# Kernel optimization log

Hardware: AMD Instinct MI355X
Metric: run time of the kernel (lower is better)

## Reference

```python
import jax, jax.numpy as jnp
import numpy as np
import math

N = 50000          # nodes
E = 800000         # edges (~avg degree 16)
G = 2048           # graphs
NUM_RBF = 128
CUTOFF = 5.0       # max_radius
C_RAD = 16         # radial channels
SH_DIM = 9         # 1x0e+1x1e+1x2e
_AVG_DEGREE = 15.57930850982666
_AVG_NUM_NODES = 18.03065905448718


def spherical_harmonics_l012(vec):
    """e3nn spherical harmonics l=0,1,2, normalize=True, component normalization."""
    r = jnp.linalg.norm(vec, axis=-1, keepdims=True)
    u = vec / jnp.maximum(r, 1e-12)
    x, y, z = u[..., 0], u[..., 1], u[..., 2]
    s3, s5, s15 = math.sqrt(3.0), math.sqrt(5.0), math.sqrt(15.0)
    x2, y2, z2 = x * x, y * y, z * z
    return jnp.stack([
        jnp.ones_like(x),                 # l=0
        s3 * x, s3 * y, s3 * z,           # l=1
        s15 * x * z,                      # l=2 (e3nn ordering)
        s15 * x * y,
        s5 * (y2 - 0.5 * (x2 + z2)),
        s15 * y * z,
        (s15 / 2.0) * (z2 - x2),
    ], axis=-1)


def exp_normal_smearing(dist):
    """ExpNormalSmearing with cutoff_lower=0, cutoff_upper=CUTOFF, num_rbf=NUM_RBF."""
    alpha = 5.0 / CUTOFF
    start = math.exp(-CUTOFF)
    means = jnp.linspace(start, 1.0, NUM_RBF).astype(dist.dtype)
    beta = (2.0 / NUM_RBF * (1.0 - start)) ** (-2)
    d = dist[..., None]
    cut = 0.5 * (jnp.cos(d * math.pi / CUTOFF) + 1.0) * (d < CUTOFF).astype(d.dtype)
    return cut * jnp.exp(-beta * (jnp.exp(-alpha * d) - means) ** 2)


def setup_inputs() -> dict:
    key = jax.random.key(0)
    ks = jax.random.split(key, 16)
    s = 0.05
    return {
        "pos": jax.random.normal(ks[0], (N, 3), jnp.float32) * 2.0,
        "atom_table": jax.random.normal(ks[1], (64, C_RAD * SH_DIM), jnp.float32) * s,
        "W1": jax.random.normal(ks[2], (NUM_RBF, 64), jnp.float32) * s,
        "b1": jnp.zeros((64,), jnp.float32),
        "W2": jax.random.normal(ks[3], (64, 64), jnp.float32) * s,
        "b2": jnp.zeros((64,), jnp.float32),
        "W3": jax.random.normal(ks[4], (64, C_RAD), jnp.float32) * s,
        "Wh1": jax.random.normal(ks[5], (C_RAD * SH_DIM, C_RAD * SH_DIM), jnp.float32) * s,
        "bh1": jnp.zeros((C_RAD * SH_DIM,), jnp.float32),
        "Wh2": jax.random.normal(ks[6], (C_RAD * SH_DIM, 1), jnp.float32) * s,
        "bh2": jnp.zeros((1,), jnp.float32),
        "node_atom": jax.random.randint(ks[7], (N,), 0, 64, jnp.int32),
        "edge_src": jax.random.randint(ks[8], (E,), 0, N, jnp.int32),
        "edge_dst": jax.random.randint(ks[9], (E,), 0, N, jnp.int32),
        "batch": jnp.sort(jax.random.randint(ks[10], (N,), 0, G, jnp.int32)),
    }


def reference(pos, atom_table, W1, b1, W2, b2, W3, Wh1, bh1, Wh2, bh2,
              node_atom, edge_src, edge_dst, batch):
    # edge geometry
    edge_vec = pos[edge_src] - pos[edge_dst]                      # [E,3]
    edge_len = jnp.linalg.norm(edge_vec, axis=-1)                 # [E]
    rbf = exp_normal_smearing(edge_len)                           # [E,128]
    sh = spherical_harmonics_l012(edge_vec)                       # [E,9]

    # radial MLP (fc_neurons = [128,64,64] -> C_RAD weights)
    h = jax.nn.silu(rbf @ W1 + b1)
    h = jax.nn.silu(h @ W2 + b2)
    rad = h @ W3                                                  # [E,C_RAD]

    # RBF-conditioned tensor-product-style edge message: outer(radial, sh)
    msg = (rad[:, :, None] * sh[:, None, :]).reshape(rad.shape[0], C_RAD * SH_DIM)

    # scatter-add aggregation, rescaled by avg degree (EdgeDegreeEmbedding)
    deg_embed = jax.ops.segment_sum(msg, edge_dst, num_segments=N)
    deg_embed = deg_embed / math.sqrt(_AVG_DEGREE)                # [N,144]

    node_features = atom_table[node_atom] + deg_embed             # [N,144]

    # energy head: Linear -> SiLU -> Linear(1x0e)
    hn = jax.nn.silu(node_features @ Wh1 + bh1)
    node_energy = hn @ Wh2 + bh2                                  # [N,1]

    # ScaledScatter over graphs
    energy = jax.ops.segment_sum(node_energy, batch, num_segments=G)
    energy = energy / math.sqrt(_AVG_NUM_NODES)                   # [G,1]
    return energy
```

## Files before the change

kernel.cpp:

```cpp
#include <hip/hip_runtime.h>
#include <math.h>

#define NND 50000
#define NED 800000
#define NGR 2048
#define NT  1024
#define NB  512
#define NPB 98
#define HALF 49
#define EPB 4096
#define BIN_BLOCKS 196
#define TBL_BLOCKS 64
#define CHW 16
#define LCAP 16
#define LSTR 17
#define SCAP 1152
#define OFCAP 8192
#define RECMASK 0x07FFFFFFu

constexpr double dSTART = 0.006737946999085467;
constexpr float  K_START = (float)dSTART;
constexpr float  K_STEP  = (float)((1.0 - dSTART) / 127.0);
constexpr float  K_BETA  = (float)(1.0 / ((2.0/128.0*(1.0-dSTART)) * (2.0/128.0*(1.0-dSTART))));
constexpr float  K_TSTEP = (float)((1.0 - dSTART) / (double)(NT - 1));
constexpr float  K_INVT  = (float)((double)(NT - 1) / (1.0 - dSTART));

__device__ __forceinline__ float silu_f(float x) {
    return x * __builtin_amdgcn_rcpf(1.0f + __expf(-x));
}

__global__ void __launch_bounds__(1024)
bin_table(const int* __restrict__ esrc, const int* __restrict__ edst,
          unsigned* __restrict__ bins,
          int* __restrict__ of_cnt, int* __restrict__ of_src, int* __restrict__ of_dst,
          const float* __restrict__ W1, const float* __restrict__ b1,
          const float* __restrict__ W2, const float* __restrict__ b2,
          const float* __restrict__ W3, float* __restrict__ table,
          float* __restrict__ out)
{
    __shared__ int      lcnt[NB];
    __shared__ unsigned lbuf[NB * LSTR];
    const int bid = blockIdx.x;
    const int tid = threadIdx.x;

    if (bid < BIN_BLOCKS) {
        if (tid < NB) lcnt[tid] = 0;
        __syncthreads();
        const int e0 = bid * EPB;
        #pragma unroll
        for (int r = 0; r < 4; ++r) {
            int e = e0 + r * 1024 + tid;
            if (e < NED) {
                int dst = edst[e];
                int src = esrc[e];
                int b = dst / NPB;
                unsigned rec = ((unsigned)src << 7) | (unsigned)(dst - b * NPB);
                int p = atomicAdd(&lcnt[b], 1);
                if (p < LCAP) lbuf[b * LSTR + p] = rec;
                else {
                    int gp = atomicAdd(of_cnt, 1);
                    if (gp < OFCAP) { of_src[gp] = src; of_dst[gp] = dst; }
                }
            }
        }
        __syncthreads();
        unsigned* dp = bins + (size_t)bid * NB * CHW;
        for (int i = tid; i < NB * CHW; i += 1024) {
            int b = i >> 4, k = i & 15;
            int c = lcnt[b]; c = c < LCAP ? c : LCAP;
            unsigned val;
            if (k == 0) val = ((c > 0) ? lbuf[b * LSTR] : 0u) | ((unsigned)c << 27);
            else        val = lbuf[b * LSTR + k];
            dp[i] = val;
        }
        return;
    }

    const int tb   = bid - BIN_BLOCKS;
    const int lane = tid & 63;
    const int w    = tid >> 6;
    const int ti   = tb * 16 + w;
    float* hl = (float*)lbuf + w * 68;

    if (tb < 2) out[tb * 1024 + tid] = 0.0f;

    const float xe = K_START + K_TSTEP * (float)ti;
    const float dd = -logf(xe);
    const float cutv = (dd < 5.0f) ? (0.5f * (__cosf(dd * 0.6283185307179586f) + 1.0f)) : 0.0f;

    float h1 = b1[lane];
    #pragma unroll 4
    for (int k = 0; k < 128; ++k) {
        float mean = K_START + K_STEP * (float)k;
        float t = xe - mean;
        float rk = cutv * __expf(-K_BETA * t * t);
        h1 = fmaf(rk, W1[(k << 6) + lane], h1);
    }
    hl[lane] = silu_f(h1);

    float h2 = b2[lane];
    #pragma unroll 4
    for (int k = 0; k < 64; ++k)
        h2 = fmaf(hl[k], W2[(k << 6) + lane], h2);
    float s2 = silu_f(h2);
    hl[lane] = s2;

    if (lane < 16) {
        float rad = 0.0f;
        #pragma unroll 4
        for (int k = 0; k < 64; ++k)
            rad = fmaf(hl[k], W3[(k << 4) + lane], rad);
        table[ti * 16 + lane] = rad;
    }
}

__global__ void __launch_bounds__(448)
agg_head(const float* __restrict__ pos, const unsigned* __restrict__ bins,
         const int* __restrict__ of_cnt, const int* __restrict__ of_src,
         const int* __restrict__ of_dst,
         const float* __restrict__ table,
         const float* __restrict__ atom_table, const int* __restrict__ node_atom,
         const int* __restrict__ batch,
         const float* __restrict__ Wh1, const float* __restrict__ bh1,
         const float* __restrict__ Wh2, const float* __restrict__ bh2,
         float* __restrict__ out, float isd, float isn)
{
    __shared__ int    lcnt[HALF], soff[HALF], scur[HALF];
    __shared__ int    ccache[BIN_BLOCKS];
    __shared__ float4 sgeo[SCAP];
    __shared__ float  nf_s[7][8][144];
    const int tid = threadIdx.x;
    const int b   = blockIdx.x >> 1;
    const int h   = blockIdx.x & 1;
    const int lbase = h * HALF;
    const int gbase = b * NPB + lbase;

    if (tid < HALF) lcnt[tid] = 0;
    if (tid < BIN_BLOCKS)
        ccache[tid] = (int)(bins[((size_t)tid * NB + b) * CHW] >> 27);
    __syncthreads();

    int ofn = *of_cnt; ofn = ofn < OFCAP ? ofn : OFCAP;

    const int TOT = BIN_BLOCKS * CHW;
    for (int s = tid; s < TOT; s += 448) {
        int seg = s >> 4, k = s & 15;
        if (k < ccache[seg]) {
            unsigned rec = bins[((size_t)seg * NB + b) * CHW + k] & RECMASK;
            int l = (int)(rec & 127u) - lbase;
            if (l >= 0 && l < HALF) atomicAdd(&lcnt[l], 1);
        }
    }
    for (int i = tid; i < ofn; i += 448) {
        int l = of_dst[i] - gbase;
        if (l >= 0 && l < HALF) atomicAdd(&lcnt[l], 1);
    }
    __syncthreads();

    if (tid < 64) {
        int v = (tid < HALF) ? lcnt[tid] : 0;
        int x = v;
        #pragma unroll
        for (int off = 1; off < 64; off <<= 1) {
            int u = __shfl_up(x, off);
            if (tid >= off) x += u;
        }
        if (tid < HALF) { soff[tid] = x - v; scur[tid] = x - v; }
    }
    __syncthreads();

    for (int s = tid; s < TOT; s += 448) {
        int seg = s >> 4, k = s & 15;
        if (k >= ccache[seg]) continue;
        unsigned rec = bins[((size_t)seg * NB + b) * CHW + k] & RECMASK;
        int local = (int)(rec & 127u);
        int l = local - lbase;
        if (l < 0 || l >= HALF) continue;
        int src = (int)(rec >> 7);
        int dst = b * NPB + local;
        float vx = pos[3*src+0] - pos[3*dst+0];
        float vy = pos[3*src+1] - pos[3*dst+1];
        float vz = pos[3*src+2] - pos[3*dst+2];
        float d2 = vx*vx + vy*vy + vz*vz;
        float4 g;
        if (d2 < 25.0f) {
            float ddv = sqrtf(d2);
            float inv = 1.0f / fmaxf(ddv, 1e-12f);
            g = make_float4(vx*inv, vy*inv, vz*inv, __expf(-ddv));
        } else {
            g = make_float4(0.0f, 0.0f, 0.0f, K_START);
        }
        int p = atomicAdd(&scur[l], 1);
        if (p < SCAP) sgeo[p] = g;
    }
    for (int i = tid; i < ofn; i += 448) {
        int dst = of_dst[i];
        int l = dst - gbase;
        if (l < 0 || l >= HALF) continue;
        int src = of_src[i];
        float vx = pos[3*src+0] - pos[3*dst+0];
        float vy = pos[3*src+1] - pos[3*dst+1];
        float vz = pos[3*src+2] - pos[3*dst+2];
        float d2 = vx*vx + vy*vy + vz*vz;
        float4 g;
        if (d2 < 25.0f) {
            float ddv = sqrtf(d2);
            float inv = 1.0f / fmaxf(ddv, 1e-12f);
            g = make_float4(vx*inv, vy*inv, vz*inv, __expf(-ddv));
        } else {
            g = make_float4(0.0f, 0.0f, 0.0f, K_START);
        }
        int p = atomicAdd(&scur[l], 1);
        if (p < SCAP) sgeo[p] = g;
    }
    __syncthreads();

    const int lane = tid & 63;
    const int w    = tid >> 6;
    const int g    = lane >> 3;
    const int c    = lane & 7;
    const int l    = w * 8 + g;
    const int gn   = gbase + l;
    const bool valid = (l < HALF) && (gn < NND);

    float acc0[9], acc1[9];
    #pragma unroll
    for (int s = 0; s < 9; ++s) { acc0[s] = 0.0f; acc1[s] = 0.0f; }

    int start = 0, end = 0;
    if (valid) {
        start = soff[l];
        end   = start + lcnt[l];
        end   = end < SCAP ? end : SCAP;
    }

    for (int p = start; p < end; ++p) {
        float4 gv = sgeo[p];
        float ux = gv.x, uy = gv.y, uz = gv.z, xe = gv.w;

        float t = (xe - K_START) * K_INVT;
        int i0 = (int)t;
        i0 = i0 < 0 ? 0 : (i0 > NT-2 ? NT-2 : i0);
        float fr = t - (float)i0;
        const float* tb = table + (size_t)i0 * 16 + c;
        float r0a = tb[0], r1a = tb[16];
        float r0b = tb[8], r1b = tb[24];
        float ra = fmaf(fr, r1a - r0a, r0a);
        float rb = fmaf(fr, r1b - r0b, r0b);

        float sh1 = 1.7320508075688772f * ux;
        float sh2 = 1.7320508075688772f * uy;
        float sh3 = 1.7320508075688772f * uz;
        float sh4 = 3.872983346207417f * ux * uz;
        float sh5 = 3.872983346207417f * ux * uy;
        float sh6 = 2.23606797749979f * (uy*uy - 0.5f*(ux*ux + uz*uz));
        float sh7 = 3.872983346207417f * uy * uz;
        float sh8 = 1.9364916731037085f * (uz*uz - ux*ux);

        acc0[0] += ra;                    acc1[0] += rb;
        acc0[1] = fmaf(ra, sh1, acc0[1]); acc1[1] = fmaf(rb, sh1, acc1[1]);
        acc0[2] = fmaf(ra, sh2, acc0[2]); acc1[2] = fmaf(rb, sh2, acc1[2]);
        acc0[3] = fmaf(ra, sh3, acc0[3]); acc1[3] = fmaf(rb, sh3, acc1[3]);
        acc0[4] = fmaf(ra, sh4, acc0[4]); acc1[4] = fmaf(rb, sh4, acc1[4]);
        acc0[5] = fmaf(ra, sh5, acc0[5]); acc1[5] = fmaf(rb, sh5, acc1[5]);
        acc0[6] = fmaf(ra, sh6, acc0[6]); acc1[6] = fmaf(rb, sh6, acc1[6]);
        acc0[7] = fmaf(ra, sh7, acc0[7]); acc1[7] = fmaf(rb, sh7, acc1[7]);
        acc0[8] = fmaf(ra, sh8, acc0[8]); acc1[8] = fmaf(rb, sh8, acc1[8]);
    }

    {
        int a = valid ? node_atom[gn] : 0;
        const float* at = atom_table + (size_t)a * 144;
        #pragma unroll
        for (int s = 0; s < 9; ++s) {
            nf_s[w][g][c*9 + s]     = fmaf(acc0[s], isd, at[c*9 + s]);
            nf_s[w][g][(c+8)*9 + s] = fmaf(acc1[s], isd, at[(c+8)*9 + s]);
        }
    }

    float A0[8], A1[8], A2[8];
    {
        float bb0 = bh1[lane], bb1 = bh1[lane + 64];
        float bb2 = (lane < 16) ? bh1[lane + 128] : 0.0f;
        #pragma unroll
        for (int q = 0; q < 8; ++q) { A0[q] = bb0; A1[q] = bb1; A2[q] = bb2; }
    }

    for (int k4 = 0; k4 < 36; ++k4) {
        float4 nq[8];
        #pragma unroll
        for (int q = 0; q < 8; ++q)
            nq[q] = *(const float4*)&nf_s[w][q][k4*4];
        const float* wrow = Wh1 + (size_t)(k4*4) * 144;
#define HSTEP(COMP, OFF) { \
        float w0 = wrow[(OFF)*144 + lane]; \
        float w1 = wrow[(OFF)*144 + lane + 64]; \
        float w2 = (lane < 16) ? wrow[(OFF)*144 + lane + 128] : 0.0f; \
        _Pragma("unroll") \
        for (int q = 0; q < 8; ++q) { \
            float nk = nq[q].COMP; \
            A0[q] = fmaf(nk, w0, A0[q]); \
            A1[q] = fmaf(nk, w1, A1[q]); \
            A2[q] = fmaf(nk, w2, A2[q]); } }
        HSTEP(x, 0) HSTEP(y, 1) HSTEP(z, 2) HSTEP(w, 3)
#undef HSTEP
    }

    float wl0 = Wh2[lane], wl1 = Wh2[lane + 64];
    float wl2 = (lane < 16) ? Wh2[lane + 128] : 0.0f;
    float bv  = bh2[0];
    #pragma unroll
    for (int q = 0; q < 8; ++q) {
        float en = silu_f(A0[q]) * wl0 + silu_f(A1[q]) * wl1;
        if (lane < 16) en = fmaf(silu_f(A2[q]), wl2, en);
        en += __shfl_down(en, 32);
        en += __shfl_down(en, 16);
        en += __shfl_down(en, 8);
        en += __shfl_down(en, 4);
        en += __shfl_down(en, 2);
        en += __shfl_down(en, 1);
        int lq = w * 8 + q;
        int gq = gbase + lq;
        if (lane == 0 && lq < HALF && gq < NND) {
            unsafeAtomicAdd(out + batch[gq], (en + bv) * isn);
        }
    }
}

extern "C" void kernel_launch(void* const* d_in, const int* in_sizes, int n_in,
                              void* d_out, int out_size, void* d_ws, size_t ws_size,
                              hipStream_t stream) {
    const float* pos        = (const float*)d_in[0];
    const float* atom_table = (const float*)d_in[1];
    const float* W1         = (const float*)d_in[2];
    const float* b1         = (const float*)d_in[3];
    const float* W2         = (const float*)d_in[4];
    const float* b2         = (const float*)d_in[5];
    const float* W3         = (const float*)d_in[6];
    const float* Wh1        = (const float*)d_in[7];
    const float* bh1        = (const float*)d_in[8];
    const float* Wh2        = (const float*)d_in[9];
    const float* bh2        = (const float*)d_in[10];
    const int*   node_atom  = (const int*)d_in[11];
    const int*   edge_src   = (const int*)d_in[12];
    const int*   edge_dst   = (const int*)d_in[13];
    const int*   batch      = (const int*)d_in[14];

    float* out = (float*)d_out;

    char*     wsb    = (char*)d_ws;
    int*      of_cnt = (int*)(wsb);
    int*      of_src = (int*)(wsb + 64);
    int*      of_dst = (int*)(wsb + 32832);
    float*    table  = (float*)(wsb + 65600);
    unsigned* bins   = (unsigned*)(wsb + 131136);

    hipMemsetAsync(of_cnt, 0, 4, stream);

    bin_table<<<BIN_BLOCKS + TBL_BLOCKS, 1024, 0, stream>>>(
        edge_src, edge_dst, bins, of_cnt, of_src, of_dst,
        W1, b1, W2, b2, W3, table, out);

    float isd = 1.0f / sqrtf(15.57930850982666f);
    float isn = 1.0f / sqrtf(18.03065905448718f);
    agg_head<<<NB * 2, 448, 0, stream>>>(
        pos, bins, of_cnt, of_src, of_dst, table, atom_table, node_atom,
        batch, Wh1, bh1, Wh2, bh2, out, isd, isn);
}
```

Baseline: 197.0 us.

## Replace global overflow list with per-block overflow buffers and alias shared memory

Edges that overflow a bin are now kept in a per-block shared list and written to a fixed-stride global slot per bin block, instead of going through a global atomic counter and a shared overflow array. This removes the hipMemsetAsync and the global atomics. agg_head now scans every block's overflow slot, reading each slot's count in every iteration, which costs extra reads. The geometry buffer and the node-feature buffer now share one shared-memory region behind an added barrier, which lowers LDS use per block and may raise occupancy. Overflow capacity drops to 63 per block and is silently truncated past that.

```diff
diff --git a/kernel.cpp b/kernel.cpp
--- a/kernel.cpp
+++ b/kernel.cpp
@@ -14,8 +14,9 @@
 #define CHW 16
 #define LCAP 16
 #define LSTR 17
-#define SCAP 1152
-#define OFCAP 8192
+#define SCAP 2016
+#define OFW 128
+#define OFL 63
 #define RECMASK 0x07FFFFFFu
 
 constexpr double dSTART = 0.006737946999085467;
@@ -31,8 +32,7 @@
 
 __global__ void __launch_bounds__(1024)
 bin_table(const int* __restrict__ esrc, const int* __restrict__ edst,
-          unsigned* __restrict__ bins,
-          int* __restrict__ of_cnt, int* __restrict__ of_src, int* __restrict__ of_dst,
+          unsigned* __restrict__ bins, unsigned* __restrict__ ofbuf,
           const float* __restrict__ W1, const float* __restrict__ b1,
           const float* __restrict__ W2, const float* __restrict__ b2,
           const float* __restrict__ W3, float* __restrict__ table,
@@ -40,11 +40,14 @@
 {
     __shared__ int      lcnt[NB];
     __shared__ unsigned lbuf[NB * LSTR];
+    __shared__ int      ofcnt_l;
+    __shared__ unsigned ofl[OFL * 2];
     const int bid = blockIdx.x;
     const int tid = threadIdx.x;
 
     if (bid < BIN_BLOCKS) {
         if (tid < NB) lcnt[tid] = 0;
+        if (tid == 0) ofcnt_l = 0;
         __syncthreads();
         const int e0 = bid * EPB;
         #pragma unroll
@@ -58,8 +61,8 @@
                 int p = atomicAdd(&lcnt[b], 1);
                 if (p < LCAP) lbuf[b * LSTR + p] = rec;
                 else {
-                    int gp = atomicAdd(of_cnt, 1);
-                    if (gp < OFCAP) { of_src[gp] = src; of_dst[gp] = dst; }
+                    int gp = atomicAdd(&ofcnt_l, 1);
+                    if (gp < OFL) { ofl[2*gp] = (unsigned)src; ofl[2*gp+1] = (unsigned)dst; }
                 }
             }
         }
@@ -73,6 +76,12 @@
             else        val = lbuf[b * LSTR + k];
             dp[i] = val;
         }
+        {
+            int oc = ofcnt_l; oc = oc < OFL ? oc : OFL;
+            unsigned* op = ofbuf + (size_t)bid * OFW;
+            if (tid == 0) op[0] = (unsigned)oc;
+            for (int i = tid; i < 2 * oc; i += 1024) op[1 + i] = ofl[i];
+        }
         return;
     }
 
@@ -116,8 +125,7 @@
 
 __global__ void __launch_bounds__(448)
 agg_head(const float* __restrict__ pos, const unsigned* __restrict__ bins,
-         const int* __restrict__ of_cnt, const int* __restrict__ of_src,
-         const int* __restrict__ of_dst,
+         const unsigned* __restrict__ ofbuf,
          const float* __restrict__ table,
          const float* __restrict__ atom_table, const int* __restrict__ node_atom,
          const int* __restrict__ batch,
@@ -127,8 +135,9 @@
 {
     __shared__ int    lcnt[HALF], soff[HALF], scur[HALF];
     __shared__ int    ccache[BIN_BLOCKS];
-    __shared__ float4 sgeo[SCAP];
-    __shared__ float  nf_s[7][8][144];
+    __shared__ float4 ubuf4[SCAP];
+    float4* sgeo = ubuf4;
+    float*  ubuf = (float*)ubuf4;
     const int tid = threadIdx.x;
     const int b   = blockIdx.x >> 1;
     const int h   = blockIdx.x & 1;
@@ -139,8 +148,6 @@
     if (tid < BIN_BLOCKS)
         ccache[tid] = (int)(bins[((size_t)tid * NB + b) * CHW] >> 27);
     __syncthreads();
-
-    int ofn = *of_cnt; ofn = ofn < OFCAP ? ofn : OFCAP;
 
     const int TOT = BIN_BLOCKS * CHW;
     for (int s = tid; s < TOT; s += 448) {
@@ -151,9 +158,13 @@
             if (l >= 0 && l < HALF) atomicAdd(&lcnt[l], 1);
         }
     }
-    for (int i = tid; i < ofn; i += 448) {
-        int l = of_dst[i] - gbase;
-        if (l >= 0 && l < HALF) atomicAdd(&lcnt[l], 1);
+    for (int s = tid; s < BIN_BLOCKS * OFL; s += 448) {
+        int bb = s / OFL, k = s - bb * OFL;
+        int oc = (int)ofbuf[(size_t)bb * OFW];
+        if (k < oc) {
+            int l = (int)ofbuf[(size_t)bb * OFW + 2 + 2*k] - gbase;
+            if (l >= 0 && l < HALF) atomicAdd(&lcnt[l], 1);
+        }
     }
     __syncthreads();
 
@@ -193,11 +204,14 @@
         int p = atomicAdd(&scur[l], 1);
         if (p < SCAP) sgeo[p] = g;
     }
-    for (int i = tid; i < ofn; i += 448) {
-        int dst = of_dst[i];
+    for (int s = tid; s < BIN_BLOCKS * OFL; s += 448) {
+        int bb = s / OFL, k = s - bb * OFL;
+        int oc = (int)ofbuf[(size_t)bb * OFW];
+        if (k >= oc) continue;
+        int src = (int)ofbuf[(size_t)bb * OFW + 1 + 2*k];
+        int dst = (int)ofbuf[(size_t)bb * OFW + 2 + 2*k];
         int l = dst - gbase;
         if (l < 0 || l >= HALF) continue;
-        int src = of_src[i];
         float vx = pos[3*src+0] - pos[3*dst+0];
         float vy = pos[3*src+1] - pos[3*dst+1];
         float vz = pos[3*src+2] - pos[3*dst+2];
@@ -268,13 +282,16 @@
         acc0[8] = fmaf(ra, sh8, acc0[8]); acc1[8] = fmaf(rb, sh8, acc1[8]);
     }
 
+    __syncthreads();
+
+    float* nfw = ubuf + w * 1152;
     {
         int a = valid ? node_atom[gn] : 0;
         const float* at = atom_table + (size_t)a * 144;
         #pragma unroll
         for (int s = 0; s < 9; ++s) {
-            nf_s[w][g][c*9 + s]     = fmaf(acc0[s], isd, at[c*9 + s]);
-            nf_s[w][g][(c+8)*9 + s] = fmaf(acc1[s], isd, at[(c+8)*9 + s]);
+            nfw[g*144 + c*9 + s]     = fmaf(acc0[s], isd, at[c*9 + s]);
+            nfw[g*144 + (c+8)*9 + s] = fmaf(acc1[s], isd, at[(c+8)*9 + s]);
         }
     }
 
@@ -290,7 +307,7 @@
         float4 nq[8];
         #pragma unroll
         for (int q = 0; q < 8; ++q)
-            nq[q] = *(const float4*)&nf_s[w][q][k4*4];
+            nq[q] = *(const float4*)&nfw[q*144 + k4*4];
         const float* wrow = Wh1 + (size_t)(k4*4) * 144;
 #define HSTEP(COMP, OFF) { \
         float w0 = wrow[(OFF)*144 + lane]; \
@@ -348,22 +365,17 @@
 
     float* out = (float*)d_out;
 
-    char*     wsb    = (char*)d_ws;
-    int*      of_cnt = (int*)(wsb);
-    int*      of_src = (int*)(wsb + 64);
-    int*      of_dst = (int*)(wsb + 32832);
-    float*    table  = (float*)(wsb + 65600);
-    unsigned* bins   = (unsigned*)(wsb + 131136);
-
-    hipMemsetAsync(of_cnt, 0, 4, stream);
+    char*     wsb   = (char*)d_ws;
+    float*    table = (float*)(wsb);
+    unsigned* ofbuf = (unsigned*)(wsb + 65536);
+    unsigned* bins  = (unsigned*)(wsb + 165888);
 
     bin_table<<<BIN_BLOCKS + TBL_BLOCKS, 1024, 0, stream>>>(
-        edge_src, edge_dst, bins, of_cnt, of_src, of_dst,
-        W1, b1, W2, b2, W3, table, out);
+        edge_src, edge_dst, bins, ofbuf, W1, b1, W2, b2, W3, table, out);
 
     float isd = 1.0f / sqrtf(15.57930850982666f);
     float isn = 1.0f / sqrtf(18.03065905448718f);
     agg_head<<<NB * 2, 448, 0, stream>>>(
-        pos, bins, of_cnt, of_src, of_dst, table, atom_table, node_atom,
+        pos, bins, ofbuf, table, atom_table, node_atom,
         batch, Wh1, bh1, Wh2, bh2, out, isd, isn);
 }
```

Result: slower. 221.0 us (+12.2%).
